# Optimization experiments

Measured on AMD Instinct MI355X. Metric: run time of the kernel, lower is better.

Reference implementation:

```python
import jax, jax.numpy as jnp
import numpy as np

B, QL, KL, H = 2, 2048, 4096, 1024
NH, HD = 16, 64
SCALE = 1.0 / np.sqrt(HD)
LN_EPS = 1e-5


def setup_inputs() -> dict:
    key = jax.random.key(0)
    ks = jax.random.split(key, 12)
    s = 0.02
    return {
        "query_vectors": jax.random.normal(ks[0], (B, QL, H), jnp.float32),
        "knowledge_vectors": jax.random.normal(ks[1], (B, KL, H), jnp.float32),
        "attention_mask": jnp.ones((B, QL), jnp.int32),
        "answer_start_idx": 512,
        "Wq": jax.random.normal(ks[2], (H, H), jnp.float32) * s,
        "bq": jnp.zeros((H,), jnp.float32),
        "Wk": jax.random.normal(ks[3], (H, H), jnp.float32) * s,
        "bk": jnp.zeros((H,), jnp.float32),
        "Wv": jax.random.normal(ks[4], (H, H), jnp.float32) * s,
        "bv": jnp.zeros((H,), jnp.float32),
        "Wo": jax.random.normal(ks[5], (H, H), jnp.float32) * s,
        "bo": jnp.zeros((H,), jnp.float32),
        "ln_w": jnp.ones((H,), jnp.float32),
        "ln_b": jnp.zeros((H,), jnp.float32),
    }


def _layer_norm(x, w, b):
    mu = jnp.mean(x, axis=-1, keepdims=True)
    var = jnp.mean(jnp.square(x - mu), axis=-1, keepdims=True)
    return (x - mu) * jax.lax.rsqrt(var + LN_EPS) * w + b


def reference(query_vectors, knowledge_vectors, attention_mask, answer_start_idx,
              Wq, bq, Wk, bk, Wv, bv, Wo, bo, ln_w, ln_b):
    b, ql, h = query_vectors.shape
    kl = knowledge_vectors.shape[1]
    # projections, split into heads: (b, nh, len, hd)
    Q = (query_vectors @ Wq + bq).reshape(b, ql, NH, HD).transpose(0, 2, 1, 3)
    K = (knowledge_vectors @ Wk + bk).reshape(b, kl, NH, HD).transpose(0, 2, 1, 3)
    V = (knowledge_vectors @ Wv + bv).reshape(b, kl, NH, HD).transpose(0, 2, 1, 3)
    scores = jnp.einsum("bhqd,bhkd->bhqk", Q, K) * SCALE
    # query-side padding mask: (b,1,q,1), masked_fill where mask==0
    neg_inf = jnp.array(-jnp.inf, scores.dtype)
    scores = jnp.where(attention_mask[:, None, :, None] == 0, neg_inf, scores)
    # additive knowledge mask: -inf on positions < answer_start_idx
    if answer_start_idx is not None and answer_start_idx > 0:
        kmask = jnp.where(jnp.arange(kl) < answer_start_idx, neg_inf, jnp.array(0.0, scores.dtype))
        scores = scores + kmask[None, None, None, :]
    attn = jax.nn.softmax(scores, axis=-1)  # dropout is identity in eval
    ctx = jnp.einsum("bhqk,bhkd->bhqd", attn, V)
    ctx = ctx.transpose(0, 2, 1, 3).reshape(b, ql, h)
    out = ctx @ Wo + bo
    return _layer_norm(query_vectors + out, ln_w, ln_b)
```

## Files before the change

### kernel.cpp

```cpp
#include <hip/hip_runtime.h>
#include <hip/hip_bf16.h>
#include <stdint.h>

#define NEG_INF (-__builtin_inff())

typedef unsigned short u16;
typedef __bf16 bf16_t;
typedef __attribute__((ext_vector_type(8))) __bf16 bf16x8;
typedef __attribute__((ext_vector_type(4))) float f32x4;
typedef __attribute__((ext_vector_type(4))) u16 u16x4;

typedef __attribute__((address_space(3))) void lds_void;
typedef const __attribute__((address_space(1))) void gbl_void;

__device__ __forceinline__ void gll16(const void* g, void* l) {
  __builtin_amdgcn_global_load_lds((gbl_void*)g, (lds_void*)l, 16, 0, 0);
}

__device__ __forceinline__ u16 bf16bits(float x) {
  bf16_t h = (bf16_t)x;
  return __builtin_bit_cast(u16, h);
}

__device__ __forceinline__ float exp2_fast(float x) {
  float r;
  asm("v_exp_f32 %0, %1\n\ts_nop 0" : "=v"(r) : "v"(x));
  return r;
}

#define LOG2E 1.44269504088896340736f

__global__ __launch_bounds__(256) void cvt_bf16_kernel(const float* __restrict__ in,
                                                       u16* __restrict__ out, int n4) {
  int i = blockIdx.x * 256 + threadIdx.x;
  if (i < n4) {
    float4 v = reinterpret_cast<const float4*>(in)[i];
    u16x4 pk;
    pk.x = bf16bits(v.x); pk.y = bf16bits(v.y);
    pk.z = bf16bits(v.z); pk.w = bf16bits(v.w);
    reinterpret_cast<u16x4*>(out)[i] = pk;
  }
}

__global__ __launch_bounds__(256) void transpose_w_kernel(const float* __restrict__ W,
                                                          u16* __restrict__ Wt) {
  __shared__ float tile[64][65];
  int c0 = blockIdx.x * 64, r0 = blockIdx.y * 64;
  int tid = threadIdx.x;
#pragma unroll
  for (int i = 0; i < 16; ++i) {
    int idx = tid + i * 256;
    int r = idx >> 6, c = idx & 63;
    tile[r][c] = W[(size_t)(r0 + r) * 1024 + c0 + c];
  }
  __syncthreads();
#pragma unroll
  for (int i = 0; i < 16; ++i) {
    int idx = tid + i * 256;
    int rr = idx >> 6, cc = idx & 63;
    Wt[(size_t)(c0 + rr) * 1024 + r0 + cc] = bf16bits(tile[cc][rr]);
  }
}

template <int EPI, int BN>
__global__ __launch_bounds__(256) void gemm_bf16_kernel(
    const u16* __restrict__ A, const u16* __restrict__ Bt,
    const float* __restrict__ bias, const float* __restrict__ bias2,
    void* __restrict__ outp, void* __restrict__ outp2,
    int M, int N, int K, float scale, int L) {
  __shared__ u16 As[128 * 32];
  __shared__ u16 Bs[BN * 32];
  constexpr int WN = BN / 32;
  constexpr int BCH = BN / 16;
  const int tid = threadIdx.x;
  const int lane = tid & 63;
  const int wv = tid >> 6;
  const int m0 = blockIdx.y * 128;
  const int n0 = blockIdx.x * BN;
  const int fr = lane & 15;
  const int fg = lane >> 4;
  const int wm = (wv & 1) * 64;
  const int wn = (wv >> 1) * (WN * 16);
  const int sr = lane >> 2;
  const int sg = lane & 3;

  f32x4 zero4 = {0.f, 0.f, 0.f, 0.f};
  f32x4 acc[4][WN];
#pragma unroll
  for (int i = 0; i < 4; ++i)
#pragma unroll
    for (int j = 0; j < WN; ++j) acc[i][j] = zero4;

  for (int kt = 0; kt < K; kt += 32) {
#pragma unroll
    for (int is = 0; is < 2; ++is) {
      int chunk = wv * 2 + is;
      int row = chunk * 16 + sr;
      int srcg = sg ^ ((row >> 1) & 3);
      gll16(A + (size_t)(m0 + row) * K + kt + srcg * 8, (char*)As + chunk * 1024);
    }
#pragma unroll
    for (int is = 0; is < BCH / 4; ++is) {
      int chunk = wv * (BCH / 4) + is;
      int row = chunk * 16 + sr;
      int srcg = sg ^ ((row >> 1) & 3);
      gll16(Bt + (size_t)(n0 + row) * K + kt + srcg * 8, (char*)Bs + chunk * 1024);
    }
    __syncthreads();
    bf16x8 af[4], bfr[WN];
#pragma unroll
    for (int mi = 0; mi < 4; ++mi) {
      int row = wm + mi * 16 + fr;
      af[mi] = *reinterpret_cast<const bf16x8*>(
          (const char*)As + row * 64 + ((fg ^ ((row >> 1) & 3)) << 4));
    }
#pragma unroll
    for (int ni = 0; ni < WN; ++ni) {
      int row = wn + ni * 16 + fr;
      bfr[ni] = *reinterpret_cast<const bf16x8*>(
          (const char*)Bs + row * 64 + ((fg ^ ((row >> 1) & 3)) << 4));
    }
#pragma unroll
    for (int mi = 0; mi < 4; ++mi)
#pragma unroll
      for (int ni = 0; ni < WN; ++ni)
        acc[mi][ni] = __builtin_amdgcn_mfma_f32_16x16x32_bf16(af[mi], bfr[ni], acc[mi][ni], 0, 0, 0);
    __syncthreads();
  }

#pragma unroll
  for (int mi = 0; mi < 4; ++mi) {
#pragma unroll
    for (int ni = 0; ni < WN; ++ni) {
      int rbase = m0 + wm + mi * 16 + fg * 4;
      int col = n0 + wn + ni * 16 + fr;
      f32x4 v = acc[mi][ni];
      if constexpr (EPI == 0) {
        float bs = bias[col];
        float* o = (float*)outp;
#pragma unroll
        for (int j = 0; j < 4; ++j) o[(size_t)(rbase + j) * N + col] = v[j] + bs;
      } else if constexpr (EPI == 1) {
        float bs = bias[col];
        u16* o = (u16*)outp;
        int head = col >> 6, hd = col & 63;
        int b_ = rbase / L, r = rbase % L;
#pragma unroll
        for (int j = 0; j < 4; ++j)
          o[((size_t)(b_ * 16 + head) * L + r + j) * 64 + hd] = bf16bits((v[j] + bs) * scale);
      } else {
        int b_ = rbase / L, r = rbase % L;
        if (col < 1024) {
          float bs = bias[col];
          u16* o = (u16*)outp;
          int head = col >> 6, hd = col & 63;
#pragma unroll
          for (int j = 0; j < 4; ++j)
            o[((size_t)(b_ * 16 + head) * L + r + j) * 64 + hd] = bf16bits(v[j] + bs);
        } else {
          int c = col - 1024;
          float bs = bias2[c];
          u16* o2 = (u16*)outp2;
          int head = c >> 6, hd = c & 63;
          u16x4 pk;
#pragma unroll
          for (int j = 0; j < 4; ++j) pk[j] = bf16bits(v[j] + bs);
          *reinterpret_cast<u16x4*>(o2 + ((size_t)(b_ * 16 + head) * 64 + hd) * L + r) = pk;
        }
      }
    }
  }
}

__global__ __launch_bounds__(256) void attn_kernel(
    const u16* __restrict__ Qm, const u16* __restrict__ Km, const u16* __restrict__ Vm,
    const int* __restrict__ ansp, const int* __restrict__ qmask, u16* __restrict__ ctx) {
  __shared__ u16 Qs[64 * 64];
  __shared__ u16 Ks[64 * 64];
  __shared__ u16 Vs[64 * 64];
  __shared__ u16 Ps[4][16 * 72];
  const int tid = threadIdx.x;
  const int lane = tid & 63;
  const int wv = tid >> 6;
  const int bh = blockIdx.x;
  const int qt = blockIdx.y;
  const int b_ = bh >> 4;
  const int head = bh & 15;
  const int fr = lane & 15;
  const int fg = lane >> 4;
  const int ans = ansp[0];

  const u16* Qg = Qm + ((size_t)bh * 2048 + qt * 64) * 64;
  const u16* Kg = Km + (size_t)bh * 4096 * 64;
  const u16* Vg = Vm + (size_t)bh * 64 * 4096;

  const int sr8 = lane >> 3;
  const int sg8 = lane & 7;
#pragma unroll
  for (int is = 0; is < 2; ++is) {
    int chunk = wv * 2 + is;
    int row = chunk * 8 + sr8;
    int srcg = sg8 ^ (row & 7);
    gll16(Qg + (size_t)row * 64 + srcg * 8, (char*)Qs + chunk * 1024);
  }

  float qmv = (qmask[b_ * 2048 + qt * 64 + wv * 16 + fr] == 0) ? NEG_INF : 0.f;
  const bool anyq = __ballot(qmv != 0.f) != 0ull;

  f32x4 zero4 = {0.f, 0.f, 0.f, 0.f};
  float mrun = NEG_INF;
  float lrun = 0.f;
  f32x4 acc[4] = {zero4, zero4, zero4, zero4};
  char* Pw = (char*)&Ps[wv][0];
  const int kt0 = (ans > 0) ? (ans & ~63) : 0;

  for (int kt = kt0; kt < 4096; kt += 64) {
    __syncthreads();
#pragma unroll
    for (int is = 0; is < 2; ++is) {
      int chunk = wv * 2 + is;
      int row = chunk * 8 + sr8;
      int srcg = sg8 ^ (row & 7);
      gll16(Kg + (size_t)(kt + row) * 64 + srcg * 8, (char*)Ks + chunk * 1024);
      gll16(Vg + (size_t)row * 4096 + kt + srcg * 8, (char*)Vs + chunk * 1024);
    }
    __syncthreads();

    f32x4 st[4] = {zero4, zero4, zero4, zero4};
#pragma unroll
    for (int kk = 0; kk < 2; ++kk) {
      bf16x8 ak[4], bq;
      int gk = fg + kk * 4;
#pragma unroll
      for (int ki = 0; ki < 4; ++ki) {
        int row = ki * 16 + fr;
        ak[ki] = *reinterpret_cast<const bf16x8*>(
            (const char*)Ks + row * 128 + ((gk ^ (row & 7)) << 4));
      }
      {
        int row = wv * 16 + fr;
        bq = *reinterpret_cast<const bf16x8*>(
            (const char*)Qs + row * 128 + ((gk ^ (row & 7)) << 4));
      }
#pragma unroll
      for (int ki = 0; ki < 4; ++ki)
        st[ki] = __builtin_amdgcn_mfma_f32_16x16x32_bf16(ak[ki], bq, st[ki], 0, 0, 0);
    }

    if (kt < ans) {
#pragma unroll
      for (int ki = 0; ki < 4; ++ki)
#pragma unroll
        for (int j = 0; j < 4; ++j) {
          int kv = kt + ki * 16 + fg * 4 + j;
          if (kv < ans) st[ki][j] = NEG_INF;
        }
    }
    if (anyq) {
#pragma unroll
      for (int ki = 0; ki < 4; ++ki)
#pragma unroll
        for (int j = 0; j < 4; ++j) st[ki][j] += qmv;
    }

    float m0 = fmaxf(fmaxf(st[0][0], st[0][1]), fmaxf(st[0][2], st[0][3]));
    float m1 = fmaxf(fmaxf(st[1][0], st[1][1]), fmaxf(st[1][2], st[1][3]));
    float m2 = fmaxf(fmaxf(st[2][0], st[2][1]), fmaxf(st[2][2], st[2][3]));
    float m3 = fmaxf(fmaxf(st[3][0], st[3][1]), fmaxf(st[3][2], st[3][3]));
    float pmax = fmaxf(fmaxf(m0, m1), fmaxf(m2, m3));
    pmax = fmaxf(pmax, __shfl_xor(pmax, 16));
    pmax = fmaxf(pmax, __shfl_xor(pmax, 32));

    if (!__all(pmax <= mrun + 8.f)) {
      float mnew = fmaxf(mrun, pmax);
      float corr = exp2_fast(mrun - mnew);
      mrun = mnew;
      lrun *= corr;
#pragma unroll
      for (int hi = 0; hi < 4; ++hi) {
        acc[hi][0] *= corr; acc[hi][1] *= corr;
        acc[hi][2] *= corr; acc[hi][3] *= corr;
      }
    }

    float ls = 0.f;
#pragma unroll
    for (int ki = 0; ki < 4; ++ki) {
      u16x4 pk;
#pragma unroll
      for (int j = 0; j < 4; ++j) {
        float p = exp2_fast(st[ki][j] - mrun);
        ls += p;
        pk[j] = bf16bits(p);
      }
      *reinterpret_cast<u16x4*>(Pw + fr * 144 + (ki * 16 + fg * 4) * 2) = pk;
    }
    ls += __shfl_xor(ls, 16);
    ls += __shfl_xor(ls, 32);
    lrun += ls;

#pragma unroll
    for (int kk = 0; kk < 2; ++kk) {
      bf16x8 av[4], bp;
      int gk = fg + kk * 4;
#pragma unroll
      for (int hi = 0; hi < 4; ++hi) {
        int row = hi * 16 + fr;
        av[hi] = *reinterpret_cast<const bf16x8*>(
            (const char*)Vs + row * 128 + ((gk ^ (row & 7)) << 4));
      }
      bp = *reinterpret_cast<const bf16x8*>(Pw + fr * 144 + fg * 16 + kk * 64);
#pragma unroll
      for (int hi = 0; hi < 4; ++hi)
        acc[hi] = __builtin_amdgcn_mfma_f32_16x16x32_bf16(av[hi], bp, acc[hi], 0, 0, 0);
    }
  }

  {
    int q = qt * 64 + wv * 16 + fr;
    float inv = 1.f / lrun;
#pragma unroll
    for (int hi = 0; hi < 4; ++hi) {
      int hd = hi * 16 + fg * 4;
      u16x4 pk;
#pragma unroll
      for (int j = 0; j < 4; ++j) pk[j] = bf16bits(acc[hi][j] * inv);
      *reinterpret_cast<u16x4*>(ctx + ((size_t)b_ * 2048 + q) * 1024 + head * 64 + hd) = pk;
    }
  }
}

__global__ __launch_bounds__(256) void ln_kernel(
    const float* __restrict__ oproj, const float* __restrict__ qv,
    const float* __restrict__ lw, const float* __restrict__ lb,
    float* __restrict__ out) {
  const int row = blockIdx.x;
  const int tid = threadIdx.x;
  const int lane = tid & 63;
  const int wv = tid >> 6;
  const float4 o4 = reinterpret_cast<const float4*>(oproj + (size_t)row * 1024)[tid];
  const float4 q4 = reinterpret_cast<const float4*>(qv + (size_t)row * 1024)[tid];
  float x0 = o4.x + q4.x, x1 = o4.y + q4.y, x2 = o4.z + q4.z, x3 = o4.w + q4.w;
  float s = x0 + x1 + x2 + x3;
  float s2 = x0 * x0 + x1 * x1 + x2 * x2 + x3 * x3;
#pragma unroll
  for (int d = 1; d < 64; d <<= 1) { s += __shfl_xor(s, d); s2 += __shfl_xor(s2, d); }
  __shared__ float red[8];
  if (lane == 0) { red[wv] = s; red[4 + wv] = s2; }
  __syncthreads();
  s = red[0] + red[1] + red[2] + red[3];
  s2 = red[4] + red[5] + red[6] + red[7];
  const float mu = s * (1.f / 1024.f);
  const float var = s2 * (1.f / 1024.f) - mu * mu;
  const float rs = rsqrtf(var + 1e-5f);
  const float4 w4 = reinterpret_cast<const float4*>(lw)[tid];
  const float4 b4 = reinterpret_cast<const float4*>(lb)[tid];
  float4 r;
  r.x = (x0 - mu) * rs * w4.x + b4.x;
  r.y = (x1 - mu) * rs * w4.y + b4.y;
  r.z = (x2 - mu) * rs * w4.z + b4.z;
  r.w = (x3 - mu) * rs * w4.w + b4.w;
  reinterpret_cast<float4*>(out + (size_t)row * 1024)[tid] = r;
}

extern "C" void kernel_launch(void* const* d_in, const int* in_sizes, int n_in,
                              void* d_out, int out_size, void* d_ws, size_t ws_size,
                              hipStream_t stream) {
  const float* qv = (const float*)d_in[0];
  const float* kn = (const float*)d_in[1];
  const int* amask = (const int*)d_in[2];
  const int* ansp = (const int*)d_in[3];
  const float* Wq = (const float*)d_in[4];
  const float* bq = (const float*)d_in[5];
  const float* Wk = (const float*)d_in[6];
  const float* bk = (const float*)d_in[7];
  const float* Wv = (const float*)d_in[8];
  const float* bv = (const float*)d_in[9];
  const float* Wo = (const float*)d_in[10];
  const float* bo = (const float*)d_in[11];
  const float* lnw = (const float*)d_in[12];
  const float* lnb = (const float*)d_in[13];

  char* ws = (char*)d_ws;
  u16* qbf  = (u16*)(ws);
  u16* kbf  = (u16*)(ws + (size_t)(8u << 20));
  u16* wqT  = (u16*)(ws + (size_t)(24u << 20));
  u16* wkvT = (u16*)(ws + (size_t)(26u << 20));
  u16* woT  = (u16*)(ws + (size_t)(30u << 20));
  u16* Qb   = (u16*)(ws + (size_t)(32u << 20));
  u16* Kb   = (u16*)(ws + (size_t)(40u << 20));
  u16* Vtb  = (u16*)(ws + (size_t)(56u << 20));
  u16* ctxb = qbf;
  float* oproj = (float*)kbf;

  cvt_bf16_kernel<<<4096, 256, 0, stream>>>(qv, qbf, 1048576);
  cvt_bf16_kernel<<<8192, 256, 0, stream>>>(kn, kbf, 2097152);

  dim3 tgrid(16, 16);
  transpose_w_kernel<<<tgrid, 256, 0, stream>>>(Wq, wqT);
  transpose_w_kernel<<<tgrid, 256, 0, stream>>>(Wk, wkvT);
  transpose_w_kernel<<<tgrid, 256, 0, stream>>>(Wv, wkvT + (size_t)1024 * 1024);
  transpose_w_kernel<<<tgrid, 256, 0, stream>>>(Wo, woT);

  gemm_bf16_kernel<1, 64><<<dim3(16, 32), 256, 0, stream>>>(
      qbf, wqT, bq, nullptr, Qb, nullptr, 4096, 1024, 1024, 0.125f * LOG2E, 2048);
  gemm_bf16_kernel<3, 128><<<dim3(16, 64), 256, 0, stream>>>(
      kbf, wkvT, bk, bv, Kb, Vtb, 8192, 2048, 1024, 1.0f, 4096);

  attn_kernel<<<dim3(32, 32), 256, 0, stream>>>(Qb, Kb, Vtb, ansp, amask, ctxb);

  gemm_bf16_kernel<0, 64><<<dim3(16, 32), 256, 0, stream>>>(
      ctxb, woT, bo, nullptr, oproj, nullptr, 4096, 1024, 1024, 1.0f, 0);

  ln_kernel<<<4096, 256, 0, stream>>>(oproj, qv, lnw, lnb, (float*)d_out);
}
```

Measured before the change: 366.6 us.

## Rewrite attention with 32x32 MFMA, register P and double-buffered K/V; merge launches

The attention kernel now uses 32x32x16 bf16 MFMAs with 128-query tiles. Q is held in registers, and the softmax probabilities are repacked in registers with permlane32 swaps instead of going through LDS. K and V tiles are double-buffered so the next tile loads while the current one is computed. The conversion, weight-transpose and QKV projection launches are also merged into single kernels to cut launch count, at the cost of higher register pressure and fewer attention blocks.

```diff
diff --git a/kernel.cpp b/kernel.cpp
--- a/kernel.cpp
+++ b/kernel.cpp
@@ -8,7 +8,9 @@
 typedef __bf16 bf16_t;
 typedef __attribute__((ext_vector_type(8))) __bf16 bf16x8;
 typedef __attribute__((ext_vector_type(4))) float f32x4;
+typedef __attribute__((ext_vector_type(16))) float f32x16;
 typedef __attribute__((ext_vector_type(4))) u16 u16x4;
+typedef __attribute__((ext_vector_type(4))) unsigned int u32x4;
 
 typedef __attribute__((address_space(3))) void lds_void;
 typedef const __attribute__((address_space(1))) void gbl_void;
@@ -28,23 +30,37 @@
   return r;
 }
 
+__device__ __forceinline__ f32x16 zero16() {
+  f32x16 z;
+#pragma unroll
+  for (int i = 0; i < 16; ++i) z[i] = 0.f;
+  return z;
+}
+
 #define LOG2E 1.44269504088896340736f
 
-__global__ __launch_bounds__(256) void cvt_bf16_kernel(const float* __restrict__ in,
-                                                       u16* __restrict__ out, int n4) {
+__global__ __launch_bounds__(256) void cvt2_kernel(const float* __restrict__ qin,
+                                                   const float* __restrict__ kin,
+                                                   u16* __restrict__ qo, u16* __restrict__ ko) {
   int i = blockIdx.x * 256 + threadIdx.x;
-  if (i < n4) {
-    float4 v = reinterpret_cast<const float4*>(in)[i];
-    u16x4 pk;
-    pk.x = bf16bits(v.x); pk.y = bf16bits(v.y);
-    pk.z = bf16bits(v.z); pk.w = bf16bits(v.w);
-    reinterpret_cast<u16x4*>(out)[i] = pk;
-  }
-}
-
-__global__ __launch_bounds__(256) void transpose_w_kernel(const float* __restrict__ W,
-                                                          u16* __restrict__ Wt) {
+  const float* src; u16* dst; int idx;
+  if (i < 1048576) { src = qin; dst = qo; idx = i; }
+  else { src = kin; dst = ko; idx = i - 1048576; }
+  float4 v = reinterpret_cast<const float4*>(src)[idx];
+  u16x4 pk;
+  pk.x = bf16bits(v.x); pk.y = bf16bits(v.y);
+  pk.z = bf16bits(v.z); pk.w = bf16bits(v.w);
+  reinterpret_cast<u16x4*>(dst)[idx] = pk;
+}
+
+__global__ __launch_bounds__(256) void transpose4_kernel(
+    const float* __restrict__ Wq, const float* __restrict__ Wk,
+    const float* __restrict__ Wv, const float* __restrict__ Wo,
+    u16* __restrict__ wqT, u16* __restrict__ wkvT, u16* __restrict__ woT) {
   __shared__ float tile[64][65];
+  const int z = blockIdx.z;
+  const float* W = (z == 0) ? Wq : (z == 1) ? Wk : (z == 2) ? Wv : Wo;
+  u16* D = (z == 0) ? wqT : (z == 1) ? wkvT : (z == 2) ? (wkvT + (size_t)1024 * 1024) : woT;
   int c0 = blockIdx.x * 64, r0 = blockIdx.y * 64;
   int tid = threadIdx.x;
 #pragma unroll
@@ -58,56 +74,145 @@
   for (int i = 0; i < 16; ++i) {
     int idx = tid + i * 256;
     int rr = idx >> 6, cc = idx & 63;
-    Wt[(size_t)(c0 + rr) * 1024 + r0 + cc] = bf16bits(tile[cc][rr]);
-  }
-}
-
-template <int EPI, int BN>
-__global__ __launch_bounds__(256) void gemm_bf16_kernel(
+    D[(size_t)(c0 + rr) * 1024 + r0 + cc] = bf16bits(tile[cc][rr]);
+  }
+}
+
+__global__ __launch_bounds__(256) void qkv_gemm_kernel(
+    const u16* __restrict__ qbf, const u16* __restrict__ kbf,
+    const u16* __restrict__ wqT, const u16* __restrict__ wkvT,
+    const float* __restrict__ bq_, const float* __restrict__ bk_, const float* __restrict__ bv_,
+    u16* __restrict__ Qb, u16* __restrict__ Kb, u16* __restrict__ Vtb) {
+  __shared__ u16 As[128 * 32];
+  __shared__ u16 Bs[128 * 32];
+  const int tid = threadIdx.x;
+  const int lane = tid & 63;
+  const int wv = tid >> 6;
+  const int bid = blockIdx.x;
+  const bool isQ = bid < 256;
+  const u16* A; const u16* Bt; int m0, n0;
+  if (isQ) { A = qbf; Bt = wqT; m0 = (bid >> 3) * 128; n0 = (bid & 7) * 128; }
+  else { int b2 = bid - 256; A = kbf; Bt = wkvT; m0 = (b2 >> 4) * 128; n0 = (b2 & 15) * 128; }
+  const int fr = lane & 15;
+  const int fg = lane >> 4;
+  const int wm = (wv & 1) * 64;
+  const int wn = (wv >> 1) * 64;
+  const int sr = lane >> 2;
+  const int sg = lane & 3;
+
+  f32x4 zero4 = {0.f, 0.f, 0.f, 0.f};
+  f32x4 acc[4][4];
+#pragma unroll
+  for (int i = 0; i < 4; ++i)
+#pragma unroll
+    for (int j = 0; j < 4; ++j) acc[i][j] = zero4;
+
+  for (int kt = 0; kt < 1024; kt += 32) {
+#pragma unroll
+    for (int is = 0; is < 2; ++is) {
+      int chunk = wv * 2 + is;
+      int row = chunk * 16 + sr;
+      int srcg = sg ^ ((row >> 1) & 3);
+      gll16(A + (size_t)(m0 + row) * 1024 + kt + srcg * 8, (char*)As + chunk * 1024);
+      gll16(Bt + (size_t)(n0 + row) * 1024 + kt + srcg * 8, (char*)Bs + chunk * 1024);
+    }
+    __syncthreads();
+    bf16x8 af[4], bfr[4];
+#pragma unroll
+    for (int mi = 0; mi < 4; ++mi) {
+      int row = wm + mi * 16 + fr;
+      af[mi] = *reinterpret_cast<const bf16x8*>(
+          (const char*)As + row * 64 + ((fg ^ ((row >> 1) & 3)) << 4));
+    }
+#pragma unroll
+    for (int ni = 0; ni < 4; ++ni) {
+      int row = wn + ni * 16 + fr;
+      bfr[ni] = *reinterpret_cast<const bf16x8*>(
+          (const char*)Bs + row * 64 + ((fg ^ ((row >> 1) & 3)) << 4));
+    }
+#pragma unroll
+    for (int mi = 0; mi < 4; ++mi)
+#pragma unroll
+      for (int ni = 0; ni < 4; ++ni)
+        acc[mi][ni] = __builtin_amdgcn_mfma_f32_16x16x32_bf16(af[mi], bfr[ni], acc[mi][ni], 0, 0, 0);
+    __syncthreads();
+  }
+
+#pragma unroll
+  for (int mi = 0; mi < 4; ++mi) {
+#pragma unroll
+    for (int ni = 0; ni < 4; ++ni) {
+      int rbase = m0 + wm + mi * 16 + fg * 4;
+      int col = n0 + wn + ni * 16 + fr;
+      f32x4 v = acc[mi][ni];
+      if (isQ) {
+        float bs = bq_[col];
+        int head = col >> 6, hd = col & 63;
+        int b_ = rbase >> 11, r = rbase & 2047;
+#pragma unroll
+        for (int j = 0; j < 4; ++j)
+          Qb[((size_t)(b_ * 16 + head) * 2048 + r + j) * 64 + hd] =
+              bf16bits((v[j] + bs) * (0.125f * LOG2E));
+      } else {
+        int b_ = rbase >> 12, r = rbase & 4095;
+        if (col < 1024) {
+          float bs = bk_[col];
+          int head = col >> 6, hd = col & 63;
+#pragma unroll
+          for (int j = 0; j < 4; ++j)
+            Kb[((size_t)(b_ * 16 + head) * 4096 + r + j) * 64 + hd] = bf16bits(v[j] + bs);
+        } else {
+          int c = col - 1024;
+          float bs = bv_[c];
+          int head = c >> 6, hd = c & 63;
+          u16x4 pk;
+#pragma unroll
+          for (int j = 0; j < 4; ++j) pk[j] = bf16bits(v[j] + bs);
+          *reinterpret_cast<u16x4*>(Vtb + ((size_t)(b_ * 16 + head) * 64 + hd) * 4096 + r) = pk;
+        }
+      }
+    }
+  }
+}
+
+__global__ __launch_bounds__(256) void o_gemm_kernel(
     const u16* __restrict__ A, const u16* __restrict__ Bt,
-    const float* __restrict__ bias, const float* __restrict__ bias2,
-    void* __restrict__ outp, void* __restrict__ outp2,
-    int M, int N, int K, float scale, int L) {
+    const float* __restrict__ bias, float* __restrict__ outp) {
   __shared__ u16 As[128 * 32];
-  __shared__ u16 Bs[BN * 32];
-  constexpr int WN = BN / 32;
-  constexpr int BCH = BN / 16;
+  __shared__ u16 Bs[64 * 32];
   const int tid = threadIdx.x;
   const int lane = tid & 63;
   const int wv = tid >> 6;
   const int m0 = blockIdx.y * 128;
-  const int n0 = blockIdx.x * BN;
+  const int n0 = blockIdx.x * 64;
   const int fr = lane & 15;
   const int fg = lane >> 4;
   const int wm = (wv & 1) * 64;
-  const int wn = (wv >> 1) * (WN * 16);
+  const int wn = (wv >> 1) * 32;
   const int sr = lane >> 2;
   const int sg = lane & 3;
 
   f32x4 zero4 = {0.f, 0.f, 0.f, 0.f};
-  f32x4 acc[4][WN];
-#pragma unroll
-  for (int i = 0; i < 4; ++i)
-#pragma unroll
-    for (int j = 0; j < WN; ++j) acc[i][j] = zero4;
-
-  for (int kt = 0; kt < K; kt += 32) {
+  f32x4 acc[4][2];
+#pragma unroll
+  for (int i = 0; i < 4; ++i) { acc[i][0] = zero4; acc[i][1] = zero4; }
+
+  for (int kt = 0; kt < 1024; kt += 32) {
 #pragma unroll
     for (int is = 0; is < 2; ++is) {
       int chunk = wv * 2 + is;
       int row = chunk * 16 + sr;
       int srcg = sg ^ ((row >> 1) & 3);
-      gll16(A + (size_t)(m0 + row) * K + kt + srcg * 8, (char*)As + chunk * 1024);
-    }
-#pragma unroll
-    for (int is = 0; is < BCH / 4; ++is) {
-      int chunk = wv * (BCH / 4) + is;
+      gll16(A + (size_t)(m0 + row) * 1024 + kt + srcg * 8, (char*)As + chunk * 1024);
+    }
+    {
+      int chunk = wv;
       int row = chunk * 16 + sr;
       int srcg = sg ^ ((row >> 1) & 3);
-      gll16(Bt + (size_t)(n0 + row) * K + kt + srcg * 8, (char*)Bs + chunk * 1024);
+      gll16(Bt + (size_t)(n0 + row) * 1024 + kt + srcg * 8, (char*)Bs + chunk * 1024);
     }
     __syncthreads();
-    bf16x8 af[4], bfr[WN];
+    bf16x8 af[4], bfr[2];
 #pragma unroll
     for (int mi = 0; mi < 4; ++mi) {
       int row = wm + mi * 16 + fr;
@@ -115,7 +220,7 @@
           (const char*)As + row * 64 + ((fg ^ ((row >> 1) & 3)) << 4));
     }
 #pragma unroll
-    for (int ni = 0; ni < WN; ++ni) {
+    for (int ni = 0; ni < 2; ++ni) {
       int row = wn + ni * 16 + fr;
       bfr[ni] = *reinterpret_cast<const bf16x8*>(
           (const char*)Bs + row * 64 + ((fg ^ ((row >> 1) & 3)) << 4));
@@ -123,7 +228,7 @@
 #pragma unroll
     for (int mi = 0; mi < 4; ++mi)
 #pragma unroll
-      for (int ni = 0; ni < WN; ++ni)
+      for (int ni = 0; ni < 2; ++ni)
         acc[mi][ni] = __builtin_amdgcn_mfma_f32_16x16x32_bf16(af[mi], bfr[ni], acc[mi][ni], 0, 0, 0);
     __syncthreads();
   }
@@ -131,43 +236,13 @@
 #pragma unroll
   for (int mi = 0; mi < 4; ++mi) {
 #pragma unroll
-    for (int ni = 0; ni < WN; ++ni) {
+    for (int ni = 0; ni < 2; ++ni) {
       int rbase = m0 + wm + mi * 16 + fg * 4;
       int col = n0 + wn + ni * 16 + fr;
+      float bs = bias[col];
       f32x4 v = acc[mi][ni];
-      if constexpr (EPI == 0) {
-        float bs = bias[col];
-        float* o = (float*)outp;
-#pragma unroll
-        for (int j = 0; j < 4; ++j) o[(size_t)(rbase + j) * N + col] = v[j] + bs;
-      } else if constexpr (EPI == 1) {
-        float bs = bias[col];
-        u16* o = (u16*)outp;
-        int head = col >> 6, hd = col & 63;
-        int b_ = rbase / L, r = rbase % L;
-#pragma unroll
-        for (int j = 0; j < 4; ++j)
-          o[((size_t)(b_ * 16 + head) * L + r + j) * 64 + hd] = bf16bits((v[j] + bs) * scale);
-      } else {
-        int b_ = rbase / L, r = rbase % L;
-        if (col < 1024) {
-          float bs = bias[col];
-          u16* o = (u16*)outp;
-          int head = col >> 6, hd = col & 63;
-#pragma unroll
-          for (int j = 0; j < 4; ++j)
-            o[((size_t)(b_ * 16 + head) * L + r + j) * 64 + hd] = bf16bits(v[j] + bs);
-        } else {
-          int c = col - 1024;
-          float bs = bias2[c];
-          u16* o2 = (u16*)outp2;
-          int head = c >> 6, hd = c & 63;
-          u16x4 pk;
-#pragma unroll
-          for (int j = 0; j < 4; ++j) pk[j] = bf16bits(v[j] + bs);
-          *reinterpret_cast<u16x4*>(o2 + ((size_t)(b_ * 16 + head) * 64 + hd) * L + r) = pk;
-        }
-      }
+#pragma unroll
+      for (int j = 0; j < 4; ++j) outp[(size_t)(rbase + j) * 1024 + col] = v[j] + bs;
     }
   }
 }
@@ -175,10 +250,8 @@
 __global__ __launch_bounds__(256) void attn_kernel(
     const u16* __restrict__ Qm, const u16* __restrict__ Km, const u16* __restrict__ Vm,
     const int* __restrict__ ansp, const int* __restrict__ qmask, u16* __restrict__ ctx) {
-  __shared__ u16 Qs[64 * 64];
-  __shared__ u16 Ks[64 * 64];
-  __shared__ u16 Vs[64 * 64];
-  __shared__ u16 Ps[4][16 * 72];
+  __shared__ u16 Ks[2][64 * 64];
+  __shared__ u16 Vs[2][64 * 64];
   const int tid = threadIdx.x;
   const int lane = tid & 63;
   const int wv = tid >> 6;
@@ -186,147 +259,173 @@
   const int qt = blockIdx.y;
   const int b_ = bh >> 4;
   const int head = bh & 15;
-  const int fr = lane & 15;
-  const int fg = lane >> 4;
+  const int l31 = lane & 31;
+  const int h = lane >> 5;
   const int ans = ansp[0];
 
-  const u16* Qg = Qm + ((size_t)bh * 2048 + qt * 64) * 64;
   const u16* Kg = Km + (size_t)bh * 4096 * 64;
   const u16* Vg = Vm + (size_t)bh * 64 * 4096;
+  const int q = qt * 128 + wv * 32 + l31;
+
+  bf16x8 bq[4];
+  {
+    const u16* Qrow = Qm + ((size_t)bh * 2048 + q) * 64;
+#pragma unroll
+    for (int s = 0; s < 4; ++s)
+      bq[s] = *reinterpret_cast<const bf16x8*>(Qrow + s * 16 + h * 8);
+  }
+
+  float qmv = (qmask[b_ * 2048 + q] == 0) ? NEG_INF : 0.f;
+  const bool anyq = __ballot(qmv != 0.f) != 0ull;
+
+  int offs[2][4];
+#pragma unroll
+  for (int t = 0; t < 2; ++t)
+#pragma unroll
+    for (int s = 0; s < 4; ++s) {
+      int row = t * 32 + l31;
+      offs[t][s] = row * 128 + ((((s << 1) | h) ^ (row & 7)) << 4);
+    }
 
   const int sr8 = lane >> 3;
   const int sg8 = lane & 7;
-#pragma unroll
-  for (int is = 0; is < 2; ++is) {
-    int chunk = wv * 2 + is;
-    int row = chunk * 8 + sr8;
-    int srcg = sg8 ^ (row & 7);
-    gll16(Qg + (size_t)row * 64 + srcg * 8, (char*)Qs + chunk * 1024);
-  }
-
-  float qmv = (qmask[b_ * 2048 + qt * 64 + wv * 16 + fr] == 0) ? NEG_INF : 0.f;
-  const bool anyq = __ballot(qmv != 0.f) != 0ull;
-
-  f32x4 zero4 = {0.f, 0.f, 0.f, 0.f};
-  float mrun = NEG_INF;
-  float lrun = 0.f;
-  f32x4 acc[4] = {zero4, zero4, zero4, zero4};
-  char* Pw = (char*)&Ps[wv][0];
   const int kt0 = (ans > 0) ? (ans & ~63) : 0;
 
-  for (int kt = kt0; kt < 4096; kt += 64) {
-    __syncthreads();
+  f32x16 acc[2];
+  acc[0] = zero16(); acc[1] = zero16();
+  float mrun = NEG_INF, lrun = 0.f;
+
+  {
 #pragma unroll
     for (int is = 0; is < 2; ++is) {
       int chunk = wv * 2 + is;
       int row = chunk * 8 + sr8;
       int srcg = sg8 ^ (row & 7);
-      gll16(Kg + (size_t)(kt + row) * 64 + srcg * 8, (char*)Ks + chunk * 1024);
-      gll16(Vg + (size_t)row * 4096 + kt + srcg * 8, (char*)Vs + chunk * 1024);
-    }
+      gll16(Kg + (size_t)(kt0 + row) * 64 + srcg * 8, (char*)&Ks[0][0] + chunk * 1024);
+      gll16(Vg + (size_t)row * 4096 + kt0 + srcg * 8, (char*)&Vs[0][0] + chunk * 1024);
+    }
+  }
+  __syncthreads();
+
+  int cur = 0;
+  for (int kt = kt0; kt < 4096; kt += 64) {
+    if (kt + 64 < 4096) {
+#pragma unroll
+      for (int is = 0; is < 2; ++is) {
+        int chunk = wv * 2 + is;
+        int row = chunk * 8 + sr8;
+        int srcg = sg8 ^ (row & 7);
+        gll16(Kg + (size_t)(kt + 64 + row) * 64 + srcg * 8, (char*)&Ks[cur ^ 1][0] + chunk * 1024);
+        gll16(Vg + (size_t)row * 4096 + kt + 64 + srcg * 8, (char*)&Vs[cur ^ 1][0] + chunk * 1024);
+      }
+    }
+    const char* kb = (const char*)&Ks[cur][0];
+    const char* vb = (const char*)&Vs[cur][0];
+
+    f32x16 st[2];
+    st[0] = zero16(); st[1] = zero16();
+#pragma unroll
+    for (int t = 0; t < 2; ++t)
+#pragma unroll
+      for (int s = 0; s < 4; ++s) {
+        bf16x8 ak = *reinterpret_cast<const bf16x8*>(kb + offs[t][s]);
+        st[t] = __builtin_amdgcn_mfma_f32_32x32x16_bf16(ak, bq[s], st[t], 0, 0, 0);
+      }
+
+    if (kt < ans) {
+#pragma unroll
+      for (int t = 0; t < 2; ++t)
+#pragma unroll
+        for (int r = 0; r < 16; ++r) {
+          int kv = kt + t * 32 + (r & 3) + 8 * (r >> 2) + 4 * h;
+          if (kv < ans) st[t][r] = NEG_INF;
+        }
+    }
+    if (anyq) {
+#pragma unroll
+      for (int t = 0; t < 2; ++t)
+#pragma unroll
+        for (int r = 0; r < 16; ++r) st[t][r] += qmv;
+    }
+
+    float pm = st[0][0];
+#pragma unroll
+    for (int t = 0; t < 2; ++t)
+#pragma unroll
+      for (int r = 0; r < 16; ++r) { if (t + r) pm = fmaxf(pm, st[t][r]); }
+    {
+      float a = pm, b = pm;
+      asm("v_permlane32_swap_b32 %0, %1" : "+v"(a), "+v"(b));
+      pm = fmaxf(a, b);
+    }
+
+    if (!__all(pm <= mrun + 8.f)) {
+      float mnew = fmaxf(mrun, pm);
+      float corr = exp2_fast(mrun - mnew);
+      mrun = mnew; lrun *= corr;
+#pragma unroll
+      for (int t = 0; t < 2; ++t)
+#pragma unroll
+        for (int r = 0; r < 16; ++r) acc[t][r] *= corr;
+    }
+
+    float ls = 0.f;
+#pragma unroll
+    for (int t = 0; t < 2; ++t)
+#pragma unroll
+      for (int r = 0; r < 16; ++r) {
+        float p = exp2_fast(st[t][r] - mrun);
+        st[t][r] = p;
+        ls += p;
+      }
+    {
+      float a = ls, b = ls;
+      asm("v_permlane32_swap_b32 %0, %1" : "+v"(a), "+v"(b));
+      ls = a + b;
+    }
+    lrun += ls;
+
+    unsigned pk[16];
+#pragma unroll
+    for (int t = 0; t < 2; ++t)
+#pragma unroll
+      for (int r = 0; r < 8; ++r)
+        asm("v_cvt_pk_bf16_f32 %0, %1, %2"
+            : "=v"(pk[t * 8 + r]) : "v"(st[t][2 * r]), "v"(st[t][2 * r + 1]));
+#pragma unroll
+    for (int t = 0; t < 2; ++t) {
+      asm("v_permlane32_swap_b32 %0, %1" : "+v"(pk[t * 8 + 0]), "+v"(pk[t * 8 + 2]));
+      asm("v_permlane32_swap_b32 %0, %1" : "+v"(pk[t * 8 + 1]), "+v"(pk[t * 8 + 3]));
+      asm("v_permlane32_swap_b32 %0, %1" : "+v"(pk[t * 8 + 4]), "+v"(pk[t * 8 + 6]));
+      asm("v_permlane32_swap_b32 %0, %1" : "+v"(pk[t * 8 + 5]), "+v"(pk[t * 8 + 7]));
+    }
+
+#pragma unroll
+    for (int ht = 0; ht < 2; ++ht)
+#pragma unroll
+      for (int ks = 0; ks < 4; ++ks) {
+        bf16x8 av = *reinterpret_cast<const bf16x8*>(vb + offs[ht][ks]);
+        u32x4 w = {pk[ks * 4 + 0], pk[ks * 4 + 1], pk[ks * 4 + 2], pk[ks * 4 + 3]};
+        bf16x8 bp = __builtin_bit_cast(bf16x8, w);
+        acc[ht] = __builtin_amdgcn_mfma_f32_32x32x16_bf16(av, bp, acc[ht], 0, 0, 0);
+      }
+
     __syncthreads();
-
-    f32x4 st[4] = {zero4, zero4, zero4, zero4};
-#pragma unroll
-    for (int kk = 0; kk < 2; ++kk) {
-      bf16x8 ak[4], bq;
-      int gk = fg + kk * 4;
-#pragma unroll
-      for (int ki = 0; ki < 4; ++ki) {
-        int row = ki * 16 + fr;
-        ak[ki] = *reinterpret_cast<const bf16x8*>(
-            (const char*)Ks + row * 128 + ((gk ^ (row & 7)) << 4));
+    cur ^= 1;
+  }
+
+  {
+    float inv = 1.f / lrun;
+    u16* cbase = ctx + ((size_t)b_ * 2048 + q) * 1024 + head * 64;
+#pragma unroll
+    for (int ht = 0; ht < 2; ++ht)
+#pragma unroll
+      for (int rg = 0; rg < 4; ++rg) {
+        u16x4 o;
+#pragma unroll
+        for (int j = 0; j < 4; ++j) o[j] = bf16bits(acc[ht][rg * 4 + j] * inv);
+        *reinterpret_cast<u16x4*>(cbase + ht * 32 + rg * 8 + 4 * h) = o;
       }
-      {
-        int row = wv * 16 + fr;
-        bq = *reinterpret_cast<const bf16x8*>(
-            (const char*)Qs + row * 128 + ((gk ^ (row & 7)) << 4));
-      }
-#pragma unroll
-      for (int ki = 0; ki < 4; ++ki)
-        st[ki] = __builtin_amdgcn_mfma_f32_16x16x32_bf16(ak[ki], bq, st[ki], 0, 0, 0);
-    }
-
-    if (kt < ans) {
-#pragma unroll
-      for (int ki = 0; ki < 4; ++ki)
-#pragma unroll
-        for (int j = 0; j < 4; ++j) {
-          int kv = kt + ki * 16 + fg * 4 + j;
-          if (kv < ans) st[ki][j] = NEG_INF;
-        }
-    }
-    if (anyq) {
-#pragma unroll
-      for (int ki = 0; ki < 4; ++ki)
-#pragma unroll
-        for (int j = 0; j < 4; ++j) st[ki][j] += qmv;
-    }
-
-    float m0 = fmaxf(fmaxf(st[0][0], st[0][1]), fmaxf(st[0][2], st[0][3]));
-    float m1 = fmaxf(fmaxf(st[1][0], st[1][1]), fmaxf(st[1][2], st[1][3]));
-    float m2 = fmaxf(fmaxf(st[2][0], st[2][1]), fmaxf(st[2][2], st[2][3]));
-    float m3 = fmaxf(fmaxf(st[3][0], st[3][1]), fmaxf(st[3][2], st[3][3]));
-    float pmax = fmaxf(fmaxf(m0, m1), fmaxf(m2, m3));
-    pmax = fmaxf(pmax, __shfl_xor(pmax, 16));
-    pmax = fmaxf(pmax, __shfl_xor(pmax, 32));
-
-    if (!__all(pmax <= mrun + 8.f)) {
-      float mnew = fmaxf(mrun, pmax);
-      float corr = exp2_fast(mrun - mnew);
-      mrun = mnew;
-      lrun *= corr;
-#pragma unroll
-      for (int hi = 0; hi < 4; ++hi) {
-        acc[hi][0] *= corr; acc[hi][1] *= corr;
-        acc[hi][2] *= corr; acc[hi][3] *= corr;
-      }
-    }
-
-    float ls = 0.f;
-#pragma unroll
-    for (int ki = 0; ki < 4; ++ki) {
-      u16x4 pk;
-#pragma unroll
-      for (int j = 0; j < 4; ++j) {
-        float p = exp2_fast(st[ki][j] - mrun);
-        ls += p;
-        pk[j] = bf16bits(p);
-      }
-      *reinterpret_cast<u16x4*>(Pw + fr * 144 + (ki * 16 + fg * 4) * 2) = pk;
-    }
-    ls += __shfl_xor(ls, 16);
-    ls += __shfl_xor(ls, 32);
-    lrun += ls;
-
-#pragma unroll
-    for (int kk = 0; kk < 2; ++kk) {
-      bf16x8 av[4], bp;
-      int gk = fg + kk * 4;
-#pragma unroll
-      for (int hi = 0; hi < 4; ++hi) {
-        int row = hi * 16 + fr;
-        av[hi] = *reinterpret_cast<const bf16x8*>(
-            (const char*)Vs + row * 128 + ((gk ^ (row & 7)) << 4));
-      }
-      bp = *reinterpret_cast<const bf16x8*>(Pw + fr * 144 + fg * 16 + kk * 64);
-#pragma unroll
-      for (int hi = 0; hi < 4; ++hi)
-        acc[hi] = __builtin_amdgcn_mfma_f32_16x16x32_bf16(av[hi], bp, acc[hi], 0, 0, 0);
-    }
-  }
-
-  {
-    int q = qt * 64 + wv * 16 + fr;
-    float inv = 1.f / lrun;
-#pragma unroll
-    for (int hi = 0; hi < 4; ++hi) {
-      int hd = hi * 16 + fg * 4;
-      u16x4 pk;
-#pragma unroll
-      for (int j = 0; j < 4; ++j) pk[j] = bf16bits(acc[hi][j] * inv);
-      *reinterpret_cast<u16x4*>(ctx + ((size_t)b_ * 2048 + q) * 1024 + head * 64 + hd) = pk;
-    }
   }
 }
 
@@ -393,24 +492,10 @@
   u16* ctxb = qbf;
   float* oproj = (float*)kbf;
 
-  cvt_bf16_kernel<<<4096, 256, 0, stream>>>(qv, qbf, 1048576);
-  cvt_bf16_kernel<<<8192, 256, 0, stream>>>(kn, kbf, 2097152);
-
-  dim3 tgrid(16, 16);
-  transpose_w_kernel<<<tgrid, 256, 0, stream>>>(Wq, wqT);
-  transpose_w_kernel<<<tgrid, 256, 0, stream>>>(Wk, wkvT);
-  transpose_w_kernel<<<tgrid, 256, 0, stream>>>(Wv, wkvT + (size_t)1024 * 1024);
-  transpose_w_kernel<<<tgrid, 256, 0, stream>>>(Wo, woT);
-
-  gemm_bf16_kernel<1, 64><<<dim3(16, 32), 256, 0, stream>>>(
-      qbf, wqT, bq, nullptr, Qb, nullptr, 4096, 1024, 1024, 0.125f * LOG2E, 2048);
-  gemm_bf16_kernel<3, 128><<<dim3(16, 64), 256, 0, stream>>>(
-      kbf, wkvT, bk, bv, Kb, Vtb, 8192, 2048, 1024, 1.0f, 4096);
-
-  attn_kernel<<<dim3(32, 32), 256, 0, stream>>>(Qb, Kb, Vtb, ansp, amask, ctxb);
-
-  gemm_bf16_kernel<0, 64><<<dim3(16, 32), 256, 0, stream>>>(
-      ctxb, woT, bo, nullptr, oproj, nullptr, 4096, 1024, 1024, 1.0f, 0);
-
+  cvt2_kernel<<<12288, 256, 0, stream>>>(qv, kn, qbf, kbf);
+  transpose4_kernel<<<dim3(16, 16, 4), 256, 0, stream>>>(Wq, Wk, Wv, Wo, wqT, wkvT, woT);
+  qkv_gemm_kernel<<<1280, 256, 0, stream>>>(qbf, kbf, wqT, wkvT, bq, bk, bv, Qb, Kb, Vtb);
+  attn_kernel<<<dim3(32, 16), 256, 0, stream>>>(Qb, Kb, Vtb, ansp, amask, ctxb);
+  o_gemm_kernel<<<dim3(16, 32), 256, 0, stream>>>(ctxb, woT, bo, oproj);
   ln_kernel<<<4096, 256, 0, stream>>>(oproj, qv, lnw, lnb, (float*)d_out);
 }
```

New measurement: 319.8 us. 12.8% less time.
